# Performance work log

Measured on AMD Instinct MI355X. Metric: run time of the kernel, lower is better.

Reference implementation:

```python
import jax, jax.numpy as jnp
import numpy as np

R = 8            # receptive_field (hardcoded r=8 in GridProcessing call)
MARGIN = 0.6     # TripletLoss(margin=0.6)
EPS = 1e-8       # F.cosine_similarity eps


def _mine_cords(B, FH, FW):
    """Replicates GridProcessing._prepare for an identity flow field
    G[b, y, x] = ((x + 0.5) / W, (y + 0.5) / H):
    at every cell center, G_xmin = x, G_xmax = x + 1, both inside bounds, and
    [x // r, (x + 1) // r + 1) = {ix}, so the positive window collapses to the
    cell itself -> anchor_cord == positive_cord == (b, ix, iy) for every cell.
    (clip(0, 31) is benign since FH = FW = 32.)
    Negative cords from _prepare are discarded by forward(), so not produced."""
    bs, ys, xs = np.meshgrid(np.arange(B), np.arange(FH), np.arange(FW), indexing='ij')
    idx = np.stack([bs, xs, ys], axis=-1).reshape(-1, 3).astype(np.int32)  # rows: (b, x, y)
    return idx, idx.copy()


def setup_inputs() -> dict:
    key = jax.random.key(0)
    B, C, FH, FW = 16, 1024, 32, 32
    k1, k2 = jax.random.split(key)
    sketch = jax.random.normal(k1, (B, C, FH, FW), dtype=jnp.float32)
    ref = jax.random.normal(k2, (B, C, FH, FW), dtype=jnp.float32)
    a_idx, p_idx = _mine_cords(B, FH, FW)
    return {
        'sketch_query_vectors': sketch,
        'ref_key_vectors': ref,
        'anchor_idx': jnp.asarray(a_idx),
        'positive_idx': jnp.asarray(p_idx),
    }


def reference(sketch_query_vectors, ref_key_vectors, anchor_idx, positive_idx):
    B, C, FH, FW = sketch_query_vectors.shape
    HW = FH * FW
    N = anchor_idx.shape[0]
    na = N // B  # anchor rows are ordered by batch index, na anchors per image

    ax = anchor_idx[:, 1].reshape(B, na)
    ay = anchor_idx[:, 2].reshape(B, na)
    # anchor = sketch[b, :, y, x]  -> (B, na, C)
    a = sketch_query_vectors[jnp.arange(B)[:, None], :, ay, ax]

    # ref_fs.view(c, h*w).permute(1, 0): row-major flatten, flat id = y*W + x
    ref_flat = ref_key_vectors.reshape(B, C, HW).transpose(0, 2, 1)  # (B, HW, C)

    # cosine similarity of every anchor vs every ref position (per batch)
    dots = jnp.einsum('bnc,bmc->bnm', a, ref_flat)          # (B, na, HW)
    a_n = jnp.linalg.norm(a, axis=-1)                        # (B, na)
    r_n = jnp.linalg.norm(ref_flat, axis=-1)                 # (B, HW)
    sim = dots / jnp.maximum(a_n[:, :, None] * r_n[:, None, :], EPS)

    # get_negative_ids: argsort(dist)[:3] -> 3 LOWEST cosine positions;
    # loss uses sum of the 3 anchor-negative cosines (broadcasted cosine sum)
    neg_sum = -jnp.sum(jax.lax.top_k(-sim, 3)[0], axis=-1)   # (B, na)

    # cos(anchor, positive) is just sim at the positive's flat position
    pos_flat = (positive_idx[:, 2] * FW + positive_idx[:, 1]).reshape(B, na)
    cos_ap = jnp.take_along_axis(sim, pos_flat[:, :, None], axis=2)[..., 0]

    # (1 - cos_ap) - (1 - neg_sum) + margin, relu, mean over the single triplet
    losses = jax.nn.relu(neg_sum - cos_ap + MARGIN)          # (B, na)
    return jnp.sum(losses) / (1e-6 + N)
```

## Files before the change

kernel.cpp:

```cpp
#include <hip/hip_runtime.h>
#include <hip/hip_bf16.h>
#include <stdint.h>

#define BATCH 16
#define CDIM  1024
#define FWID  32
#define HW    1024
#define NA    1024
#define NTOT  (BATCH*NA)
#define NCHUNK 16
#define MARGIN 0.6f

typedef __bf16 bf16x8 __attribute__((ext_vector_type(8)));
typedef float  f32x4  __attribute__((ext_vector_type(4)));
typedef unsigned short us4 __attribute__((ext_vector_type(4)));
typedef unsigned short us8 __attribute__((ext_vector_type(8)));
typedef float  f4     __attribute__((ext_vector_type(4)));

template<int OFF>
__device__ __forceinline__ us4 tr_read(uint32_t addr){
  us4 r;
  asm volatile("ds_read_b64_tr_b16 %0, %1 offset:%2" : "=v"(r) : "v"(addr), "n"(OFF));
  return r;
}

__device__ __forceinline__ void gload16(const unsigned short* g, unsigned short* l){
  __builtin_amdgcn_global_load_lds((const __attribute__((address_space(1))) void*)g,
                                   (__attribute__((address_space(3))) void*)l, 16, 0, 0);
}

union FragU  { us4 h[2]; bf16x8 v; };
union FragU8 { us8 u;    bf16x8 v; };

__device__ __forceinline__ void ins3(float& a, float& b, float& c, float v){
  if (v < c){
    c = v;
    if (c < b){ float t=b; b=c; c=t;
      if (b < a){ t=a; a=b; b=t; }
    }
  }
}

#define MFMA __builtin_amdgcn_mfma_f32_16x16x32_bf16

__global__ __launch_bounds__(256)
void convert_transpose3(const float* __restrict__ S, const float* __restrict__ R,
                        unsigned short* __restrict__ tS, unsigned short* __restrict__ tR,
                        float* __restrict__ pnorm){
  const int blk = blockIdx.x;
  const int e   = blk >> 10;
  const int b   = (blk >> 6) & 15;
  const int hwT = (blk >> 2) & 15;
  const int cP  = blk & 3;
  const float* src = (e ? R : S) + (size_t)b*CDIM*HW;
  unsigned short* dst = (e ? tR : tS) + (size_t)b*HW*CDIM;

  const int t   = threadIdx.x;
  const int cj  = t & 15;
  const int hwg = t >> 4;
  const int hw0 = hwT*64 + hwg*4;
  const int cA  = cP*256 + cj*8;
  const int cB  = cA + 128;

  f4 colA[8], colB[8];
  #pragma unroll
  for (int i = 0; i < 8; ++i)
    colA[i] = *(const f4*)&src[(size_t)(cA + i)*HW + hw0];
  #pragma unroll
  for (int i = 0; i < 8; ++i)
    colB[i] = *(const f4*)&src[(size_t)(cB + i)*HW + hw0];

  float sqa[4] = {0.f,0.f,0.f,0.f};
  float sqb[4] = {0.f,0.f,0.f,0.f};
  #pragma unroll
  for (int j = 0; j < 4; ++j){
    us8 pk;
    float sq = 0.f;
    #pragma unroll
    for (int i = 0; i < 8; ++i){
      __hip_bfloat16 h = __float2bfloat16(colA[i][j]);
      pk[i] = __builtin_bit_cast(unsigned short, h);
      const float g = __bfloat162float(h);
      sq = fmaf(g, g, sq);
    }
    *(us8*)&dst[(size_t)(hw0 + j)*CDIM + cA] = pk;
    sqa[j] = sq;
  }
  #pragma unroll
  for (int j = 0; j < 4; ++j){
    us8 pk;
    float sq = 0.f;
    #pragma unroll
    for (int i = 0; i < 8; ++i){
      __hip_bfloat16 h = __float2bfloat16(colB[i][j]);
      pk[i] = __builtin_bit_cast(unsigned short, h);
      const float g = __bfloat162float(h);
      sq = fmaf(g, g, sq);
    }
    *(us8*)&dst[(size_t)(hw0 + j)*CDIM + cB] = pk;
    sqb[j] = sq;
  }
  #pragma unroll
  for (int m = 1; m < 16; m <<= 1){
    #pragma unroll
    for (int j = 0; j < 4; ++j){
      sqa[j] += __shfl_xor(sqa[j], m);
      sqb[j] += __shfl_xor(sqb[j], m);
    }
  }
  if (cj == 0){
    f4 oa = {sqa[0], sqa[1], sqa[2], sqa[3]};
    f4 ob = {sqb[0], sqb[1], sqb[2], sqb[3]};
    *(f4*)&pnorm[((size_t)(e*16 + b)*8 + cP*2    )*HW + hw0] = oa;
    *(f4*)&pnorm[((size_t)(e*16 + b)*8 + cP*2 + 1)*HW + hw0] = ob;
  }
}

__global__ __launch_bounds__(256)
void norm_reduce(const float* __restrict__ pnorm, float* __restrict__ snorm){
  const int eb = blockIdx.x;
  const int t  = threadIdx.x;
  #pragma unroll
  for (int r = 0; r < 4; ++r){
    const int hw = r*256 + t;
    float a = 0.f;
    #pragma unroll
    for (int ct = 0; ct < 8; ++ct)
      a += pnorm[((size_t)eb*8 + ct)*HW + hw];
    snorm[(size_t)eb*HW + hw] = sqrtf(a);
  }
}

__global__ __launch_bounds__(512, 2)
void fused_gemm_top3_v9(const unsigned short* __restrict__ tS,
                        const unsigned short* __restrict__ tR,
                        const float* __restrict__ snorm,
                        const int*   __restrict__ anchor,
                        const int*   __restrict__ posidx,
                        float* __restrict__ wtop,
                        float* __restrict__ wpos)
{
  __shared__ unsigned short stage[65536];
  __shared__ int   p_lds[256], q_lds[256];
  __shared__ float nAs[256], nBs[256];

  const int t = threadIdx.x;
  const uint32_t bid = blockIdx.x;
  const uint32_t L = (bid & 7u)*32u + (bid >> 3);
  const int b  = L >> 4;
  const int ni = (L >> 2) & 3;
  const int mi = L & 3;

  const unsigned short* SbT = tS + (size_t)b*HW*CDIM;
  const unsigned short* RbT = tR + (size_t)b*HW*CDIM;

  if (t < 256){
    const int n_g = ni*256 + t;
    const int* ap = anchor + (size_t)(b*NA + n_g)*3;
    const int* pp = posidx + (size_t)(b*NA + n_g)*3;
    const int pv = ap[2]*FWID + ap[1];
    p_lds[t] = pv;
    q_lds[t] = pp[2]*FWID + pp[1];
    nAs[t] = 1.0f / snorm[(size_t)b*HW + pv];
  } else {
    nBs[t-256] = 1.0f / snorm[(size_t)(BATCH + b)*HW + mi*256 + (t-256)];
  }
  __syncthreads();

  const int l  = t & 63;
  const int w  = t >> 6;
  const int wr = w >> 2, wc = w & 3;

  const int gkc = (l&7) ^ ((l>>3)&7);
  const unsigned short* gA[4];
  const unsigned short* gB[4];
  #pragma unroll
  for (int i = 0; i < 4; ++i){
    const int row = w*32 + i*8 + (l>>3);
    gA[i] = SbT + (size_t)p_lds[row]*CDIM + gkc*8;
    gB[i] = RbT + (size_t)(mi*256 + row)*CDIM + gkc*8;
  }
  unsigned short* lA = &stage[w*2048];
  unsigned short* lB = &stage[32768 + w*2048];

  const int fb0 = (l&15)*64 + (((l>>4)    ) ^ (l&7))*8;
  const int fb1 = (l&15)*64 + (((l>>4) + 4) ^ (l&7))*8;
  const int abase = wr*8192;
  const int bbase = 32768 + wc*4096;

  f32x4 acc[8][4];
  #pragma unroll
  for (int i=0;i<8;i++){
    #pragma unroll
    for (int j=0;j<4;j++){ f32x4 z = {0.f,0.f,0.f,0.f}; acc[i][j] = z; }
  }

  auto stage8 = [&](int bo, int kt){
    const int ko = kt*64;
    #pragma unroll
    for (int i = 0; i < 4; ++i){
      gload16(gA[i] + ko, lA + bo + i*512);
      gload16(gB[i] + ko, lB + bo + i*512);
    }
  };

  auto half = [&](int bo, int fbh){
    FragU8 Bf[4], Af[8];
    #pragma unroll
    for (int fb=0; fb<4; ++fb) Bf[fb].u = *(const us8*)&stage[bbase + bo + fb*1024 + fbh];
    #pragma unroll
    for (int fa=0; fa<8; ++fa) Af[fa].u = *(const us8*)&stage[abase + bo + fa*1024 + fbh];
    __builtin_amdgcn_s_setprio(1);
    #pragma unroll
    for (int fa=0; fa<8; ++fa){
      #pragma unroll
      for (int fb=0; fb<4; ++fb)
        acc[fa][fb] = MFMA(Af[fa].v, Bf[fb].v, acc[fa][fb], 0,0,0);
    }
    __builtin_amdgcn_s_setprio(0);
  };

  stage8(0, 0);
  int bo = 0;
  for (int kt = 0; kt < 16; ++kt){
    asm volatile("s_waitcnt vmcnt(0)" ::: "memory");
    __builtin_amdgcn_s_barrier();
    __builtin_amdgcn_sched_barrier(0);
    if (kt < 15) stage8(bo ^ 16384, kt+1);
    half(bo, fb0);
    half(bo, fb1);
    bo ^= 16384;
  }

  __syncthreads();
  float* tls = (float*)&stage[0] + (size_t)w*1152;

  float rinv[4];
  #pragma unroll
  for (int fb=0; fb<4; ++fb) rinv[fb] = nBs[wc*64 + fb*16 + (l&15)];

  #pragma unroll
  for (int fa=0; fa<8; ++fa){
    #pragma unroll
    for (int r=0; r<4; ++r){
      const int rg    = (l>>4)*4 + r;
      const int row_l = wr*128 + fa*16 + rg;
      const float ain = nAs[row_l];
      const float v0 = acc[fa][0][r] * ain * rinv[0];
      const float v1 = acc[fa][1][r] * ain * rinv[1];
      const float v2 = acc[fa][2][r] * ain * rinv[2];
      const float v3 = acc[fa][3][r] * ain * rinv[3];

      const int n_g = ni*256 + row_l;
      const int q   = q_lds[row_l];
      const int ql  = q - (mi*256 + wc*64);
      if (ql >= 0 && ql < 64 && (ql & 15) == (l & 15)){
        const int sel = ql >> 4;
        const float pv = sel==0 ? v0 : sel==1 ? v1 : sel==2 ? v2 : v3;
        wpos[b*NA + n_g] = pv;
      }

      float x=1e30f, y=1e30f, z=1e30f;
      ins3(x,y,z,v0); ins3(x,y,z,v1); ins3(x,y,z,v2); ins3(x,y,z,v3);
      f4 tr = {x, y, z, 0.f};
      *(f4*)(tls + (rg*17 + (l&15))*4) = tr;
    }
    asm volatile("s_waitcnt lgkmcnt(0)" ::: "memory");
    __builtin_amdgcn_sched_barrier(0);

    {
      const int rr = l >> 2;
      const float* rbp = tls + (rr*17 + (l&3)*4)*4;
      const f4 t0 = *(const f4*)(rbp);
      const f4 t1 = *(const f4*)(rbp + 4);
      const f4 t2 = *(const f4*)(rbp + 8);
      const f4 t3 = *(const f4*)(rbp + 12);
      float x = t0[0], y = t0[1], z = t0[2];
      ins3(x,y,z,t1[0]); ins3(x,y,z,t1[1]); ins3(x,y,z,t1[2]);
      ins3(x,y,z,t2[0]); ins3(x,y,z,t2[1]); ins3(x,y,z,t2[2]);
      ins3(x,y,z,t3[0]); ins3(x,y,z,t3[1]); ins3(x,y,z,t3[2]);
      #pragma unroll
      for (int m=1; m<4; m<<=1){
        const float ox = __shfl_xor(x, m);
        const float oy = __shfl_xor(y, m);
        const float oz = __shfl_xor(z, m);
        ins3(x,y,z,ox); ins3(x,y,z,oy); ins3(x,y,z,oz);
      }
      if ((l & 3) == 0){
        const int n_g = ni*256 + wr*128 + fa*16 + rr;
        float* dst = wtop + ((size_t)(b*NA + n_g)*NCHUNK + (mi*4 + wc))*3;
        dst[0]=x; dst[1]=y; dst[2]=z;
      }
    }
    asm volatile("s_waitcnt lgkmcnt(0)" ::: "memory");
    __builtin_amdgcn_sched_barrier(0);
  }
}

__global__ __launch_bounds__(256)
void fused_gemm_top3_v1(const float* __restrict__ sketch,
                        const float* __restrict__ refk,
                        const int*   __restrict__ anchor,
                        const int*   __restrict__ posidx,
                        float* __restrict__ wtop,
                        float* __restrict__ wpos)
{
  __shared__ union {
    unsigned short stage[16384];
    struct { float nA[16][128]; float nB[16][128]; } nrm;
  } sh;
  __shared__ int   p_lds[128];
  __shared__ float nA2[128], nB2[128];

  const int t = threadIdx.x;
  const uint32_t bid = blockIdx.x;
  const uint32_t L = (bid & 7u)*128u + (bid >> 3);
  const int b  = L >> 6;
  const int ni = (L >> 3) & 7;
  const int mi = L & 7;

  const float* Sb = sketch + (size_t)b*CDIM*HW;
  const float* Rb = refk   + (size_t)b*CDIM*HW;

  if (t < 128){
    const int n_g = ni*128 + t;
    const int* ap = anchor + (size_t)(b*NA + n_g)*3;
    p_lds[t] = ap[2]*FWID + ap[1];
  }
  __syncthreads();
  const int p0 = p_lds[0];
  int okf = 1;
  if (t < 128) okf = (p_lds[t] == p0 + t);
  const int contig = __syncthreads_and(okf);

  const int colg = (t & 15)*8;
  const int rowg = t >> 4;
  const int mbase = mi*128;

  const int l  = t & 63;
  const int w  = t >> 6;
  const int wr = w >> 1, wc = w & 1;
  const uint32_t sh_base = (uint32_t)(uintptr_t)&sh.stage[0];
  const uint32_t laneA = ((uint32_t)(l>>4))*2048u + (uint32_t)wr*512u + (uint32_t)(l&15)*8u;
  const uint32_t laneB = ((uint32_t)(l>>4))*2048u + (uint32_t)wc*512u + (uint32_t)(l&15)*8u;
  const int off0 = ((rowg>>2)*8 + (colg>>4))*64 + (rowg&3)*16 + (colg&15);

  f32x4 acc[4][4];
  #pragma unroll
  for (int i=0;i<4;i++){
    #pragma unroll
    for (int j=0;j<4;j++){ f32x4 z = {0.f,0.f,0.f,0.f}; acc[i][j] = z; }
  }

  float sqA[8] = {0,0,0,0,0,0,0,0};
  float sqB[8] = {0,0,0,0,0,0,0,0};
  f4 ra[4], rb[4];

  auto load_tile = [&](int kt){
    const int c0 = kt*32 + rowg;
    const float* SA = Sb + (size_t)c0*HW;
    const float* RB = Rb + (size_t)c0*HW + mbase + colg;
    if (contig){
      const float* pA = SA + p0 + colg;
      ra[0] = *(const f4*)(pA);
      ra[1] = *(const f4*)(pA + 4);
      ra[2] = *(const f4*)(pA + 16*HW);
      ra[3] = *(const f4*)(pA + 16*HW + 4);
    } else {
      float* raf = (float*)ra;
      #pragma unroll
      for (int i=0;i<8;i++){
        const int pc = p_lds[colg + i];
        raf[i]   = SA[pc];
        raf[8+i] = SA[16*HW + pc];
      }
    }
    rb[0] = *(const f4*)(RB);
    rb[1] = *(const f4*)(RB + 4);
    rb[2] = *(const f4*)(RB + 16*HW);
    rb[3] = *(const f4*)(RB + 16*HW + 4);
  };

  auto cvt_store = [&](int buf){
    const float* raf = (const float*)ra;
    const float* rbf = (const float*)rb;
    us8 pk;
    #pragma unroll
    for (int i=0;i<8;i++){
      __hip_bfloat16 h = __float2bfloat16(raf[i]);
      pk[i] = __builtin_bit_cast(unsigned short, h);
      const float g = __bfloat162float(h);
      sqA[i] = fmaf(g, g, sqA[i]);
    }
    *(us8*)&sh.stage[buf*4096 + off0] = pk;
    #pragma unroll
    for (int i=0;i<8;i++){
      __hip_bfloat16 h = __float2bfloat16(raf[8+i]);
      pk[i] = __builtin_bit_cast(unsigned short, h);
      const float g = __bfloat162float(h);
      sqA[i] = fmaf(g, g, sqA[i]);
    }
    *(us8*)&sh.stage[buf*4096 + off0 + 2048] = pk;
    #pragma unroll
    for (int i=0;i<8;i++){
      __hip_bfloat16 h = __float2bfloat16(rbf[i]);
      pk[i] = __builtin_bit_cast(unsigned short, h);
      const float g = __bfloat162float(h);
      sqB[i] = fmaf(g, g, sqB[i]);
    }
    *(us8*)&sh.stage[8192 + buf*4096 + off0] = pk;
    #pragma unroll
    for (int i=0;i<8;i++){
      __hip_bfloat16 h = __float2bfloat16(rbf[8+i]);
      pk[i] = __builtin_bit_cast(unsigned short, h);
      const float g = __bfloat162float(h);
      sqB[i] = fmaf(g, g, sqB[i]);
    }
    *(us8*)&sh.stage[8192 + buf*4096 + off0 + 2048] = pk;
  };

  auto compute = [&](int buf){
    const uint32_t aaddr = sh_base + (uint32_t)buf*8192u + laneA;
    const uint32_t baddr = sh_base + 16384u + (uint32_t)buf*8192u + laneB;
    FragU A0,A1,A2,A3,B0,B1,B2,B3;
    A0.h[0]=tr_read<0>(aaddr);    A0.h[1]=tr_read<1024>(aaddr);
    A1.h[0]=tr_read<128>(aaddr);  A1.h[1]=tr_read<1152>(aaddr);
    A2.h[0]=tr_read<256>(aaddr);  A2.h[1]=tr_read<1280>(aaddr);
    A3.h[0]=tr_read<384>(aaddr);  A3.h[1]=tr_read<1408>(aaddr);
    B0.h[0]=tr_read<0>(baddr);    B0.h[1]=tr_read<1024>(baddr);
    B1.h[0]=tr_read<128>(baddr);  B1.h[1]=tr_read<1152>(baddr);
    B2.h[0]=tr_read<256>(baddr);  B2.h[1]=tr_read<1280>(baddr);
    B3.h[0]=tr_read<384>(baddr);  B3.h[1]=tr_read<1408>(baddr);
    asm volatile("s_waitcnt lgkmcnt(0)" ::: "memory");
    __builtin_amdgcn_sched_barrier(0);
    acc[0][0]=MFMA(A0.v,B0.v,acc[0][0],0,0,0);
    acc[0][1]=MFMA(A0.v,B1.v,acc[0][1],0,0,0);
    acc[0][2]=MFMA(A0.v,B2.v,acc[0][2],0,0,0);
    acc[0][3]=MFMA(A0.v,B3.v,acc[0][3],0,0,0);
    acc[1][0]=MFMA(A1.v,B0.v,acc[1][0],0,0,0);
    acc[1][1]=MFMA(A1.v,B1.v,acc[1][1],0,0,0);
    acc[1][2]=MFMA(A1.v,B2.v,acc[1][2],0,0,0);
    acc[1][3]=MFMA(A1.v,B3.v,acc[1][3],0,0,0);
    acc[2][0]=MFMA(A2.v,B0.v,acc[2][0],0,0,0);
    acc[2][1]=MFMA(A2.v,B1.v,acc[2][1],0,0,0);
    acc[2][2]=MFMA(A2.v,B2.v,acc[2][2],0,0,0);
    acc[2][3]=MFMA(A2.v,B3.v,acc[2][3],0,0,0);
    acc[3][0]=MFMA(A3.v,B0.v,acc[3][0],0,0,0);
    acc[3][1]=MFMA(A3.v,B1.v,acc[3][1],0,0,0);
    acc[3][2]=MFMA(A3.v,B2.v,acc[3][2],0,0,0);
    acc[3][3]=MFMA(A3.v,B3.v,acc[3][3],0,0,0);
  };

  load_tile(0);
  cvt_store(0);
  __syncthreads();
  int buf = 0;
  for (int kt = 0; kt < 32; ++kt){
    if (kt < 31) load_tile(kt+1);
    compute(buf);
    if (kt < 31) cvt_store(buf^1);
    __syncthreads();
    buf ^= 1;
  }

  #pragma unroll
  for (int i=0;i<8;i++) sh.nrm.nA[rowg][colg+i] = sqA[i];
  #pragma unroll
  for (int i=0;i<8;i++) sh.nrm.nB[rowg][colg+i] = sqB[i];
  __syncthreads();
  if (t < 128){
    float s = 0.f;
    #pragma unroll
    for (int r=0;r<16;r++) s += sh.nrm.nA[r][t];
    nA2[t] = s;
  } else {
    const int c2 = t - 128;
    float s = 0.f;
    #pragma unroll
    for (int r=0;r<16;r++) s += sh.nrm.nB[r][c2];
    nB2[c2] = s;
  }
  __syncthreads();

  float rncol[4];
  #pragma unroll
  for (int nf=0;nf<4;nf++) rncol[nf] = sqrtf(nB2[wc*64 + nf*16 + (l&15)]);

  #pragma unroll
  for (int mf=0; mf<4; ++mf){
    #pragma unroll
    for (int r=0; r<4; ++r){
      const int row_l = wr*64 + mf*16 + (l>>4)*4 + r;
      const int n_g   = ni*128 + row_l;
      const float an  = sqrtf(nA2[row_l]);
      const float v0 = acc[mf][0][r] / fmaxf(an*rncol[0], 1e-8f);
      const float v1 = acc[mf][1][r] / fmaxf(an*rncol[1], 1e-8f);
      const float v2 = acc[mf][2][r] / fmaxf(an*rncol[2], 1e-8f);
      const float v3 = acc[mf][3][r] / fmaxf(an*rncol[3], 1e-8f);

      const int* pp = posidx + (size_t)(b*NA + n_g)*3;
      const int q  = pp[2]*FWID + pp[1];
      const int ql = q - (mbase + wc*64);
      if (ql >= 0 && ql < 64 && (ql & 15) == (l & 15)){
        const int sel = ql >> 4;
        const float pv = sel==0 ? v0 : sel==1 ? v1 : sel==2 ? v2 : v3;
        wpos[b*NA + n_g] = pv;
      }

      float x=1e30f, y=1e30f, z=1e30f;
      ins3(x,y,z,v0); ins3(x,y,z,v1); ins3(x,y,z,v2); ins3(x,y,z,v3);
      #pragma unroll
      for (int m=1; m<16; m<<=1){
        const float ox = __shfl_xor(x, m);
        const float oy = __shfl_xor(y, m);
        const float oz = __shfl_xor(z, m);
        ins3(x,y,z,ox); ins3(x,y,z,oy); ins3(x,y,z,oz);
      }
      if ((l & 15) == 0){
        float* dst = wtop + ((size_t)(b*NA + n_g)*NCHUNK + (mi*2 + wc))*3;
        dst[0]=x; dst[1]=y; dst[2]=z;
      }
    }
  }
}

__global__ __launch_bounds__(256)
void merge_top3(const float* __restrict__ wtop, const float* __restrict__ wpos,
                float* __restrict__ partial){
  __shared__ float red[256];
  const int id = blockIdx.x*256 + threadIdx.x;
  const float* src = wtop + (size_t)id*(NCHUNK*3);
  float x=1e30f, y=1e30f, z=1e30f;
  #pragma unroll
  for (int i=0;i<NCHUNK*3;i++) ins3(x,y,z, src[i]);
  const float loss = fmaxf((x+y+z) - wpos[id] + MARGIN, 0.0f);
  red[threadIdx.x] = loss;
  __syncthreads();
  for (int s=128; s>0; s>>=1){
    if (threadIdx.x < s) red[threadIdx.x] += red[threadIdx.x+s];
    __syncthreads();
  }
  if (threadIdx.x == 0) partial[blockIdx.x] = red[0];
}

__global__ void final_sum(const float* __restrict__ partial, float* __restrict__ out){
  float v = partial[threadIdx.x];
  #pragma unroll
  for (int off=32; off>0; off>>=1) v += __shfl_down(v, off);
  if (threadIdx.x == 0) out[0] = v / (1e-6f + (float)NTOT);
}

extern "C" void kernel_launch(void* const* d_in, const int* in_sizes, int n_in,
                              void* d_out, int out_size, void* d_ws, size_t ws_size,
                              hipStream_t stream){
  const float* sketch = (const float*)d_in[0];
  const float* refk   = (const float*)d_in[1];
  const int*   anchor = (const int*)d_in[2];
  const int*   posidx = (const int*)d_in[3];
  float* out = (float*)d_out;

  float* wtop    = (float*)d_ws;
  float* wpos    = wtop + (size_t)NTOT*NCHUNK*3;
  float* partial = wpos + NTOT;
  unsigned short* tS = (unsigned short*)(partial + 256);
  unsigned short* tR = tS + (size_t)BATCH*HW*CDIM;
  float* pnorm = (float*)(tR + (size_t)BATCH*HW*CDIM);
  float* snorm = pnorm + (size_t)32*8*1024;
  const size_t need = (size_t)((char*)(snorm + 32*1024) - (char*)d_ws);

  if (ws_size >= need){
    convert_transpose3<<<dim3(2048), dim3(256), 0, stream>>>(sketch, refk, tS, tR, pnorm);
    norm_reduce<<<dim3(32), dim3(256), 0, stream>>>(pnorm, snorm);
    fused_gemm_top3_v9<<<dim3(256), dim3(512), 0, stream>>>(tS, tR, snorm, anchor, posidx, wtop, wpos);
  } else {
    fused_gemm_top3_v1<<<dim3(1024), dim3(256), 0, stream>>>(sketch, refk, anchor, posidx, wtop, wpos);
  }
  merge_top3<<<dim3(64), dim3(256), 0, stream>>>(wtop, wpos, partial);
  final_sum<<<dim3(1), dim3(64), 0, stream>>>(partial, out);
}
```

Measured before the change: 97.25 us.

## Fuse norm reduction into convert-transpose and stage transposed rows through LDS

The bf16 convert/transpose kernel now has each 512-thread block cover all 1024 channels for 64 spatial positions. It stages the transposed tile in shared memory and writes full contiguous 2KB rows to global memory instead of scattered 16-byte chunks. Because each block now sees every channel for its positions, it finishes the squared-norm reduction itself, which removes the pnorm buffer and the separate norm_reduce launch. The cost is a large shared-memory footprint (about 140KB per block), so fewer blocks can be resident, and the grid shrinks from 2048 to 512 blocks.

```diff
diff --git a/kernel.cpp b/kernel.cpp
--- a/kernel.cpp
+++ b/kernel.cpp
@@ -43,91 +43,70 @@
 
 #define MFMA __builtin_amdgcn_mfma_f32_16x16x32_bf16
 
-__global__ __launch_bounds__(256)
-void convert_transpose3(const float* __restrict__ S, const float* __restrict__ R,
+__global__ __launch_bounds__(512)
+void convert_transpose4(const float* __restrict__ S, const float* __restrict__ R,
                         unsigned short* __restrict__ tS, unsigned short* __restrict__ tR,
-                        float* __restrict__ pnorm){
+                        float* __restrict__ snorm){
+  __shared__ unsigned short tile[64*1032];
+  __shared__ float nsq[64][33];
+
   const int blk = blockIdx.x;
-  const int e   = blk >> 10;
-  const int b   = (blk >> 6) & 15;
-  const int hwT = (blk >> 2) & 15;
-  const int cP  = blk & 3;
+  const int e   = blk >> 8;
+  const int b   = (blk >> 4) & 15;
+  const int hwT = blk & 15;
   const float* src = (e ? R : S) + (size_t)b*CDIM*HW;
   unsigned short* dst = (e ? tR : tS) + (size_t)b*HW*CDIM;
 
-  const int t   = threadIdx.x;
-  const int cj  = t & 15;
-  const int hwg = t >> 4;
-  const int hw0 = hwT*64 + hwg*4;
-  const int cA  = cP*256 + cj*8;
-  const int cB  = cA + 128;
-
-  f4 colA[8], colB[8];
-  #pragma unroll
-  for (int i = 0; i < 8; ++i)
-    colA[i] = *(const f4*)&src[(size_t)(cA + i)*HW + hw0];
-  #pragma unroll
-  for (int i = 0; i < 8; ++i)
-    colB[i] = *(const f4*)&src[(size_t)(cB + i)*HW + hw0];
-
-  float sqa[4] = {0.f,0.f,0.f,0.f};
-  float sqb[4] = {0.f,0.f,0.f,0.f};
-  #pragma unroll
-  for (int j = 0; j < 4; ++j){
-    us8 pk;
-    float sq = 0.f;
-    #pragma unroll
-    for (int i = 0; i < 8; ++i){
-      __hip_bfloat16 h = __float2bfloat16(colA[i][j]);
-      pk[i] = __builtin_bit_cast(unsigned short, h);
-      const float g = __bfloat162float(h);
-      sq = fmaf(g, g, sq);
-    }
-    *(us8*)&dst[(size_t)(hw0 + j)*CDIM + cA] = pk;
-    sqa[j] = sq;
-  }
-  #pragma unroll
-  for (int j = 0; j < 4; ++j){
-    us8 pk;
-    float sq = 0.f;
-    #pragma unroll
-    for (int i = 0; i < 8; ++i){
-      __hip_bfloat16 h = __float2bfloat16(colB[i][j]);
-      pk[i] = __builtin_bit_cast(unsigned short, h);
-      const float g = __bfloat162float(h);
-      sq = fmaf(g, g, sq);
-    }
-    *(us8*)&dst[(size_t)(hw0 + j)*CDIM + cB] = pk;
-    sqb[j] = sq;
-  }
-  #pragma unroll
-  for (int m = 1; m < 16; m <<= 1){
+  const int t  = threadIdx.x;
+  const int li = t & 15;
+  const int gi = t >> 4;
+  const int hwb = hwT*64 + li*4;
+
+  float sq0=0.f, sq1=0.f, sq2=0.f, sq3=0.f;
+  #pragma unroll
+  for (int it = 0; it < 4; ++it){
+    const int cb = it*256 + gi*8;
+    f4 col[8];
+    #pragma unroll
+    for (int i = 0; i < 8; ++i)
+      col[i] = *(const f4*)&src[(size_t)(cb + i)*HW + hwb];
     #pragma unroll
     for (int j = 0; j < 4; ++j){
-      sqa[j] += __shfl_xor(sqa[j], m);
-      sqb[j] += __shfl_xor(sqb[j], m);
-    }
-  }
-  if (cj == 0){
-    f4 oa = {sqa[0], sqa[1], sqa[2], sqa[3]};
-    f4 ob = {sqb[0], sqb[1], sqb[2], sqb[3]};
-    *(f4*)&pnorm[((size_t)(e*16 + b)*8 + cP*2    )*HW + hw0] = oa;
-    *(f4*)&pnorm[((size_t)(e*16 + b)*8 + cP*2 + 1)*HW + hw0] = ob;
-  }
-}
-
-__global__ __launch_bounds__(256)
-void norm_reduce(const float* __restrict__ pnorm, float* __restrict__ snorm){
-  const int eb = blockIdx.x;
-  const int t  = threadIdx.x;
-  #pragma unroll
-  for (int r = 0; r < 4; ++r){
-    const int hw = r*256 + t;
+      us8 pk;
+      float sq = 0.f;
+      #pragma unroll
+      for (int i = 0; i < 8; ++i){
+        __hip_bfloat16 h = __float2bfloat16(col[i][j]);
+        pk[i] = __builtin_bit_cast(unsigned short, h);
+        const float g = __bfloat162float(h);
+        sq = fmaf(g, g, sq);
+      }
+      *(us8*)&tile[(li*4 + j)*1032 + cb] = pk;
+      if (j==0) sq0+=sq; else if (j==1) sq1+=sq; else if (j==2) sq2+=sq; else sq3+=sq;
+    }
+  }
+  nsq[li*4+0][gi] = sq0;
+  nsq[li*4+1][gi] = sq1;
+  nsq[li*4+2][gi] = sq2;
+  nsq[li*4+3][gi] = sq3;
+  __syncthreads();
+
+  const int w = t >> 6, l = t & 63;
+  #pragma unroll
+  for (int rr = 0; rr < 8; ++rr){
+    const int row = w*8 + rr;
+    const us8 v0 = *(const us8*)&tile[row*1032 + l*8];
+    const us8 v1 = *(const us8*)&tile[row*1032 + 512 + l*8];
+    unsigned short* drow = dst + (size_t)(hwT*64 + row)*CDIM;
+    *(us8*)(drow + l*8)       = v0;
+    *(us8*)(drow + 512 + l*8) = v1;
+  }
+
+  if (t < 64){
     float a = 0.f;
     #pragma unroll
-    for (int ct = 0; ct < 8; ++ct)
-      a += pnorm[((size_t)eb*8 + ct)*HW + hw];
-    snorm[(size_t)eb*HW + hw] = sqrtf(a);
+    for (int g2 = 0; g2 < 32; ++g2) a += nsq[t][g2];
+    snorm[(size_t)(e*16 + b)*HW + hwT*64 + t] = sqrtf(a);
   }
 }
 
@@ -564,13 +543,11 @@
   float* partial = wpos + NTOT;
   unsigned short* tS = (unsigned short*)(partial + 256);
   unsigned short* tR = tS + (size_t)BATCH*HW*CDIM;
-  float* pnorm = (float*)(tR + (size_t)BATCH*HW*CDIM);
-  float* snorm = pnorm + (size_t)32*8*1024;
+  float* snorm = (float*)(tR + (size_t)BATCH*HW*CDIM);
   const size_t need = (size_t)((char*)(snorm + 32*1024) - (char*)d_ws);
 
   if (ws_size >= need){
-    convert_transpose3<<<dim3(2048), dim3(256), 0, stream>>>(sketch, refk, tS, tR, pnorm);
-    norm_reduce<<<dim3(32), dim3(256), 0, stream>>>(pnorm, snorm);
+    convert_transpose4<<<dim3(512), dim3(512), 0, stream>>>(sketch, refk, tS, tR, snorm);
     fused_gemm_top3_v9<<<dim3(256), dim3(512), 0, stream>>>(tS, tR, snorm, anchor, posidx, wtop, wpos);
   } else {
     fused_gemm_top3_v1<<<dim3(1024), dim3(256), 0, stream>>>(sketch, refk, anchor, posidx, wtop, wpos);
```

Measured after the change: 95.16 us (median of 2 runs). 2.2% less time.
